# Kernel tuning notes

Hardware: AMD Instinct MI355X
Metric: run time of the kernel (lower is better)

The kernel has to match this reference:

```python
import jax, jax.numpy as jnp
import numpy as np
import math

D_MODEL = 1024
N_HEADS = 16
D_K = D_MODEL // N_HEADS
THRESH = 0.1  # attention probs below this are zeroed


def setup_inputs() -> dict:
    key = jax.random.key(0)
    ks = jax.random.split(key, 9)
    B, S, D = 2, 2048, D_MODEL
    scale = 1.0 / math.sqrt(D)
    x = jax.random.normal(ks[0], (B, S, D), dtype=jnp.float32)
    Wq = jax.random.normal(ks[1], (D, D), dtype=jnp.float32) * scale
    bq = jax.random.normal(ks[2], (D,), dtype=jnp.float32) * 0.01
    Wk = jax.random.normal(ks[3], (D, D), dtype=jnp.float32) * scale
    bk = jax.random.normal(ks[4], (D,), dtype=jnp.float32) * 0.01
    Wv = jax.random.normal(ks[5], (D, D), dtype=jnp.float32) * scale
    bv = jax.random.normal(ks[6], (D,), dtype=jnp.float32) * 0.01
    Wo = jax.random.normal(ks[7], (D, D), dtype=jnp.float32) * scale
    bo = jax.random.normal(ks[8], (D,), dtype=jnp.float32) * 0.01
    return {"x": x, "Wq": Wq, "bq": bq, "Wk": Wk, "bk": bk,
            "Wv": Wv, "bv": bv, "Wo": Wo, "bo": bo}


def _split_heads(t):
    B, S, D = t.shape
    return t.reshape(B, S, N_HEADS, D_K).transpose(0, 2, 1, 3)  # [B,H,S,dk]


def reference(x, Wq, bq, Wk, bk, Wv, bv, Wo, bo):
    # torch nn.Linear: y = x @ W.T + b
    q = _split_heads(x @ Wq.T + bq)
    k = _split_heads(x @ Wk.T + bk)
    v = _split_heads(x @ Wv.T + bv)
    scores = jnp.einsum('bhqd,bhkd->bhqk', q, k) / math.sqrt(D_K)
    probs = jax.nn.softmax(scores, axis=-1)          # full unmasked softmax (returned)
    keep = probs >= THRESH                            # ~low_attention_mask
    probs_model = jnp.where(keep, probs, 0.0)        # masked_fill; dropout is identity in eval
    ctx = jnp.einsum('bhqk,bhkd->bhqd', probs_model, v)
    B, H, S, dk = ctx.shape
    merged = ctx.transpose(0, 2, 1, 3).reshape(B, S, H * dk)
    out = merged @ Wo.T + bo
    attention_sum = probs.sum(axis=1)                # [B,S,S] sum over heads
    attention_mask = keep.astype(jnp.float32).sum(axis=1)  # [B,S,S]
    return (out, attention_sum, attention_mask)
```

## Files before the change

kernel.cpp:

```cpp
#include <hip/hip_runtime.h>

#define SDIM 2048
#define DDIM 1024
#define NH 16
#define DK 64
#define NB 2
#define MROWS (NB * SDIM)
#define MAXEV 65536
#define EXPC 0.18033688011112f
#define L01 -3.3219281f

typedef _Float16 f16x8 __attribute__((ext_vector_type(8)));
typedef _Float16 f16x4 __attribute__((ext_vector_type(4)));
typedef float f32x4 __attribute__((ext_vector_type(4)));

__device__ __forceinline__ void ld_lds16(const _Float16* g, _Float16* l) {
  __builtin_amdgcn_global_load_lds(
      (const __attribute__((address_space(1))) void*)g,
      (__attribute__((address_space(3))) void*)l, 16, 0, 0);
}

__global__ __launch_bounds__(256) void cvt_f16(
    const float* __restrict__ x, const float* __restrict__ wq,
    const float* __restrict__ wk, const float* __restrict__ wv,
    _Float16* __restrict__ xh, _Float16* __restrict__ wqh,
    _Float16* __restrict__ wkh, _Float16* __restrict__ wvh) {
  int i = blockIdx.x * 256 + threadIdx.x;
  const float* src;
  _Float16* dst;
  int off;
  if (i < 1048576) {
    src = x; dst = xh; off = i;
  } else if (i < 1310720) {
    src = wq; dst = wqh; off = i - 1048576;
  } else if (i < 1572864) {
    src = wk; dst = wkh; off = i - 1310720;
  } else {
    src = wv; dst = wvh; off = i - 1572864;
  }
  float4 v = ((const float4*)src)[off];
  f16x4 h;
  h[0] = (_Float16)v.x; h[1] = (_Float16)v.y;
  h[2] = (_Float16)v.z; h[3] = (_Float16)v.w;
  ((f16x4*)dst)[off] = h;
}

__global__ __launch_bounds__(256, 2) void proj_gemm(
    const _Float16* __restrict__ xh, const _Float16* __restrict__ Wqh,
    const _Float16* __restrict__ Wkh, const _Float16* __restrict__ Wvh,
    const float* __restrict__ bq, const float* __restrict__ bk,
    const float* __restrict__ bv, _Float16* __restrict__ Qo,
    _Float16* __restrict__ Ko, float* __restrict__ Vo) {
  __shared__ _Float16 sA[128 * 64];
  __shared__ _Float16 sB[128 * 64];
  const int t = threadIdx.x;
  const int lane = t & 63, wv = t >> 6;
  const int lr = lane & 15, quad = lane >> 4;
  const int wm = wv >> 1, wn = wv & 1;
  const int m0 = blockIdx.y * 128, n0 = blockIdx.x * 128;
  const int z = blockIdx.z;
  const _Float16* Bp = z == 0 ? Wqh : (z == 1 ? Wkh : Wvh);
  const float* bias = z == 0 ? bq : (z == 1 ? bk : bv);

  const int strow = t >> 3;
  const int stchunk = t & 7;
  const int stsrc = (stchunk ^ (strow & 7)) * 8;

  f32x4 acc[4][4];
#pragma unroll
  for (int i = 0; i < 4; ++i)
#pragma unroll
    for (int j = 0; j < 4; ++j) acc[i][j] = (f32x4){0.f, 0.f, 0.f, 0.f};

  for (int k0 = 0; k0 < DDIM; k0 += 64) {
    __syncthreads();
#pragma unroll
    for (int i = 0; i < 4; ++i) {
      const int row = i * 32 + strow;
      ld_lds16(&xh[(size_t)(m0 + row) * DDIM + k0 + stsrc],
               &sA[row * 64 + stchunk * 8]);
      ld_lds16(&Bp[(size_t)(n0 + row) * DDIM + k0 + stsrc],
               &sB[row * 64 + stchunk * 8]);
    }
    __syncthreads();
    f16x8 af[4][2], bf[4][2];
#pragma unroll
    for (int i = 0; i < 4; ++i)
#pragma unroll
      for (int kk = 0; kk < 2; ++kk) {
        const int ph = ((kk * 4 + quad) ^ (lr & 7)) * 8;
        af[i][kk] = *(const f16x8*)&sA[(wm * 64 + i * 16 + lr) * 64 + ph];
        bf[i][kk] = *(const f16x8*)&sB[(wn * 64 + i * 16 + lr) * 64 + ph];
      }
#pragma unroll
    for (int kk = 0; kk < 2; ++kk)
#pragma unroll
      for (int i = 0; i < 4; ++i)
#pragma unroll
        for (int j = 0; j < 4; ++j)
          acc[i][j] = __builtin_amdgcn_mfma_f32_16x16x32_f16(
              af[i][kk], bf[j][kk], acc[i][j], 0, 0, 0);
  }
#pragma unroll
  for (int j = 0; j < 4; ++j) {
    const int ng = n0 + wn * 64 + j * 16 + lr;
    const float bvv = bias[ng];
    const int h = ng >> 6, d = ng & 63;
#pragma unroll
    for (int i = 0; i < 4; ++i) {
#pragma unroll
      for (int r = 0; r < 4; ++r) {
        const int mg = m0 + wm * 64 + i * 16 + quad * 4 + r;
        const int b = mg >> 11, s = mg & 2047;
        const float o = acc[i][j][r] + bvv;
        const size_t off = ((size_t)(b * NH + h) * SDIM + s) * DK + d;
        if (z == 0)
          Qo[off] = (_Float16)(o * EXPC);
        else if (z == 1)
          Ko[off] = (_Float16)o;
        else
          Vo[off] = o;
      }
    }
  }
}

__global__ __launch_bounds__(256, 8) void attn_denom(
    const _Float16* __restrict__ Q, const _Float16* __restrict__ K,
    float* __restrict__ laOut) {
  __shared__ _Float16 KdA[64 * 64];
  __shared__ _Float16 KdB[64 * 64];
  const int t = threadIdx.x;
  const int lane = t & 63, wave = t >> 6;
  const int quad = lane >> 4, lr = lane & 15;
  const int id = blockIdx.x;
  const int xcd = id & 7, inner = id >> 3;
  const int bh = xcd * 4 + (inner >> 5);
  const int q0 = (inner & 31) * 64;
  const _Float16* Qh = Q + (size_t)bh * SDIM * DK;
  const _Float16* Kh = K + (size_t)bh * SDIM * DK;
  const size_t qoff = (size_t)(q0 + wave * 16 + lr) * DK + quad * 8;
  const f16x8 aq0 = *(const f16x8*)&Qh[qoff];
  const f16x8 aq1 = *(const f16x8*)&Qh[qoff + 32];
  const int strow = t >> 3, stchunk = t & 7;
  const int stsrc = (stchunk ^ (strow & 7)) * 8;
  const int ph0 = (quad ^ (lr & 7)) * 8;
  const int ph1 = ((4 + quad) ^ (lr & 7)) * 8;

#define STAGE_DN(KT, BUF)                                                  \
  {                                                                        \
    _Pragma("unroll") for (int i = 0; i < 2; ++i)                          \
        ld_lds16(&Kh[(size_t)((KT)*64 + i * 32 + strow) * DK + stsrc],     \
                 &BUF[(i * 32 + strow) * 64 + stchunk * 8]);               \
  }

#define COMPUTE_DN(BUF)                                                   \
  _Pragma("unroll") for (int c = 0; c < 4; ++c) {                         \
    f16x8 b0 = *(const f16x8*)&BUF[(c * 16 + lr) * 64 + ph0];             \
    f16x8 b1 = *(const f16x8*)&BUF[(c * 16 + lr) * 64 + ph1];             \
    f32x4 acc = {0.f, 0.f, 0.f, 0.f};                                     \
    acc = __builtin_amdgcn_mfma_f32_16x16x32_f16(aq0, b0, acc, 0, 0, 0);  \
    acc = __builtin_amdgcn_mfma_f32_16x16x32_f16(aq1, b1, acc, 0, 0, 0);  \
    _Pragma("unroll") for (int r = 0; r < 4; ++r)                         \
        dsum[r] += __builtin_amdgcn_exp2f(acc[r]);                        \
  }

  float dsum[4] = {0.f, 0.f, 0.f, 0.f};
  STAGE_DN(0, KdA);
#pragma unroll 1
  for (int kt = 0; kt < 32; kt += 2) {
    __syncthreads();
    STAGE_DN(kt + 1, KdB);
    COMPUTE_DN(KdA);
    __syncthreads();
    if (kt + 2 < 32) STAGE_DN(kt + 2, KdA);
    COMPUTE_DN(KdB);
  }
#pragma unroll
  for (int m = 1; m < 16; m <<= 1)
#pragma unroll
    for (int r = 0; r < 4; ++r)
      dsum[r] += __shfl_xor(dsum[r], m, 64);
  if (lr == 0) {
#pragma unroll
    for (int r = 0; r < 4; ++r)
      laOut[(size_t)bh * SDIM + q0 + wave * 16 + quad * 4 + r] =
          -__builtin_amdgcn_logf(dsum[r]);
  }
#undef STAGE_DN
#undef COMPUTE_DN
}

__global__ __launch_bounds__(256, 6) void attn_pass2(
    const _Float16* __restrict__ Q, const _Float16* __restrict__ K,
    const float* __restrict__ la, float* __restrict__ attSum,
    float* __restrict__ attMask, float4* __restrict__ ev,
    int* __restrict__ ecnt) {
  __shared__ __align__(16) float SMEM[64 * 68];
  _Float16* KbufA = (_Float16*)SMEM;
  _Float16* KbufB = (_Float16*)SMEM + 4096;
  float* Tbuf = SMEM;
  const int t = threadIdx.x;
  const int lane = t & 63, wave = t >> 6;
  const int quad = lane >> 4, lr = lane & 15;
  const int id = blockIdx.x;
  const int xcd = id & 7, inner = id >> 3;
  const int b = xcd >> 2;
  const int q0 = (((xcd >> 1) & 1) * 16 + (inner >> 4)) * 64;
  const int k0 = ((xcd & 1) * 16 + (inner & 15)) * 64;
  const int strow = t >> 3, stchunk = t & 7;
  const int stsrc = (stchunk ^ (strow & 7)) * 8;
  const int ph0 = (quad ^ (lr & 7)) * 8;
  const int ph1 = ((4 + quad) ^ (lr & 7)) * 8;

  const size_t qbase = ((size_t)(b * NH) * SDIM + q0 + wave * 16 + lr) * DK;
  const size_t dbase = (size_t)(b * NH) * SDIM + q0 + wave * 16 + quad * 4;
  const size_t hstep = (size_t)SDIM * DK;

  float asum[4][4] = {};
  float mxr[4] = {-1e30f, -1e30f, -1e30f, -1e30f};

  f16x8 aq0c, aq1c, aq0n, aq1n;
  float4 lavc, lavn;

#define STAGE_H(H, BUF)                                                      \
  {                                                                          \
    const _Float16* Kp =                                                     \
        K + (size_t)(b * NH + (H)) * hstep + (size_t)k0 * DK;                \
    _Pragma("unroll") for (int i = 0; i < 2; ++i)                            \
        ld_lds16(&Kp[(size_t)(i * 32 + strow) * DK + stsrc],                 \
                 &BUF[(i * 32 + strow) * 64 + stchunk * 8]);                 \
  }

#define LOADQ_H(H, A0, A1, LV)                                               \
  {                                                                          \
    const size_t ho = (size_t)(H)*hstep;                                     \
    A0 = *(const f16x8*)&Q[qbase + ho + quad * 8];                           \
    A1 = *(const f16x8*)&Q[qbase + ho + 32 + quad * 8];                      \
    LV = *(const float4*)&la[dbase + (size_t)(H)*SDIM];                      \
  }

#define COMPUTE_H(BUF, A0, A1, LV)                                           \
  {                                                                          \
    const float lar[4] = {LV.x, LV.y, LV.z, LV.w};                           \
    _Pragma("unroll") for (int c = 0; c < 4; ++c) {                          \
      f16x8 b0 = *(const f16x8*)&BUF[(c * 16 + lr) * 64 + ph0];              \
      f16x8 b1 = *(const f16x8*)&BUF[(c * 16 + lr) * 64 + ph1];              \
      f32x4 acc = {0.f, 0.f, 0.f, 0.f};                                      \
      acc = __builtin_amdgcn_mfma_f32_16x16x32_f16(A0, b0, acc, 0, 0, 0);    \
      acc = __builtin_amdgcn_mfma_f32_16x16x32_f16(A1, b1, acc, 0, 0, 0);    \
      _Pragma("unroll") for (int r = 0; r < 4; ++r) {                        \
        const float arg = acc[r] + lar[r];                                   \
        mxr[r] = fmaxf(mxr[r], arg);                                         \
        asum[c][r] += __builtin_amdgcn_exp2f(arg);                           \
      }                                                                      \
    }                                                                        \
  }

  STAGE_H(0, KbufA);
  LOADQ_H(0, aq0c, aq1c, lavc);
#pragma unroll 1
  for (int h = 0; h < NH; h += 2) {
    __syncthreads();
    STAGE_H(h + 1, KbufB);
    LOADQ_H(h + 1, aq0n, aq1n, lavn);
    COMPUTE_H(KbufA, aq0c, aq1c, lavc);
    __syncthreads();
    if (h + 2 < NH) {
      STAGE_H(h + 2, KbufA);
      LOADQ_H(h + 2, aq0c, aq1c, lavc);
    }
    COMPUTE_H(KbufB, aq0n, aq1n, lavn);
  }
#undef STAGE_H
#undef LOADQ_H
#undef COMPUTE_H

  const float mx =
      fmaxf(fmaxf(mxr[0], mxr[1]), fmaxf(mxr[2], mxr[3]));
  if (__any(mx >= L01)) {
    float amask[4][4] = {};
#pragma unroll 1
    for (int h = 0; h < NH; ++h) {
      const _Float16* Kp =
          K + (size_t)(b * NH + h) * hstep + (size_t)k0 * DK;
      const size_t ho = (size_t)h * hstep;
      const f16x8 aq0 = *(const f16x8*)&Q[qbase + ho + quad * 8];
      const f16x8 aq1 = *(const f16x8*)&Q[qbase + ho + 32 + quad * 8];
      const float4 l4 = *(const float4*)&la[dbase + (size_t)h * SDIM];
      const float lar[4] = {l4.x, l4.y, l4.z, l4.w};
#pragma unroll 1
      for (int c = 0; c < 4; ++c) {
        const f16x8 b0 = *(const f16x8*)&Kp[(c * 16 + lr) * DK + quad * 8];
        const f16x8 b1 = *(const f16x8*)&Kp[(c * 16 + lr) * DK + 32 + quad * 8];
        f32x4 acc = {0.f, 0.f, 0.f, 0.f};
        acc = __builtin_amdgcn_mfma_f32_16x16x32_f16(aq0, b0, acc, 0, 0, 0);
        acc = __builtin_amdgcn_mfma_f32_16x16x32_f16(aq1, b1, acc, 0, 0, 0);
#pragma unroll 1
        for (int r = 0; r < 4; ++r) {
          const float p = __builtin_amdgcn_exp2f(acc[r] + lar[r]);
          if (p >= 0.1f) {
            amask[c][r] += 1.0f;
            int idx = atomicAdd(ecnt, 1);
            if (idx < MAXEV)
              ev[idx] = make_float4(
                  __int_as_float(b * NH + h),
                  __int_as_float(q0 + wave * 16 + quad * 4 + r),
                  __int_as_float(k0 + c * 16 + lr), p);
          }
        }
      }
    }
#pragma unroll
    for (int c = 0; c < 4; ++c)
#pragma unroll
      for (int r = 0; r < 4; ++r)
        if (amask[c][r] != 0.0f) {
          const size_t row = (size_t)(b * SDIM) + q0 + wave * 16 + quad * 4 + r;
          attMask[row * SDIM + k0 + c * 16 + lr] = amask[c][r];
        }
  }
  const int g8 = t >> 3;
  const int l8 = (t & 7) * 4;
  __syncthreads();
#pragma unroll
  for (int c = 0; c < 4; ++c)
#pragma unroll
    for (int r = 0; r < 4; ++r)
      Tbuf[(wave * 16 + quad * 4 + r) * 68 + c * 16 + lr] = asum[c][r];
  __syncthreads();
#pragma unroll
  for (int p = 0; p < 2; ++p)
#pragma unroll
    for (int qh = 0; qh < 2; ++qh) {
      const int row = p * 32 + g8, col = qh * 32 + l8;
      f32x4 v = *(const f32x4*)&Tbuf[row * 68 + col];
      __builtin_nontemporal_store(
          v, (f32x4*)&attSum[((size_t)(b * SDIM) + q0 + row) * SDIM + k0 + col]);
    }
}

__global__ __launch_bounds__(64) void apply_events(
    const float4* __restrict__ ev, const int* __restrict__ ecnt,
    const float* __restrict__ V, float* __restrict__ merged,
    int* __restrict__ flags) {
  int n = *ecnt;
  if (n > MAXEV) n = MAXEV;
  const int d = threadIdx.x;
  for (int e = blockIdx.x; e < n; e += gridDim.x) {
    float4 r = ev[e];
    int bh = __float_as_int(r.x);
    int q = __float_as_int(r.y);
    int kc = __float_as_int(r.z);
    float p = r.w;
    int b = bh >> 4, h = bh & 15;
    atomicAdd(&merged[((size_t)(b * SDIM + q)) * DDIM + h * DK + d],
              p * V[((size_t)bh * SDIM + kc) * DK + d]);
    if (d == 0) flags[b * SDIM + q] = 1;
  }
}

__global__ __launch_bounds__(256) void out_gemm(const float* __restrict__ A,
                                                const float* __restrict__ W,
                                                const float* __restrict__ bias,
                                                float* __restrict__ out,
                                                const int* __restrict__ flags) {
  __shared__ float As[16][68];
  __shared__ float Ws[16][68];
  __shared__ int anyF;
  const int t = threadIdx.x;
  const int tx = t & 15, ty = t >> 4;
  const int m0 = blockIdx.y * 64;
  const int n0 = blockIdx.x * 64;
  if (t == 0) anyF = 0;
  __syncthreads();
  if (t < 64 && flags[m0 + t]) anyF = 1;
  __syncthreads();
  const int nb = n0 + tx * 4;
  const float4 bv = *(const float4*)&bias[nb];
  if (!anyF) {
#pragma unroll
    for (int r = 0; r < 4; ++r)
      *(float4*)&out[(size_t)(m0 + ty * 4 + r) * DDIM + nb] = bv;
    return;
  }
  const int lr = t >> 2;
  const int lc = (t & 3) * 4;
  float acc[4][4] = {};
  for (int k0 = 0; k0 < DDIM; k0 += 16) {
    __syncthreads();
    float4 av = *(const float4*)&A[(size_t)(m0 + lr) * DDIM + k0 + lc];
    float4 wv = *(const float4*)&W[(size_t)(n0 + lr) * DDIM + k0 + lc];
    As[lc + 0][lr] = av.x; As[lc + 1][lr] = av.y;
    As[lc + 2][lr] = av.z; As[lc + 3][lr] = av.w;
    Ws[lc + 0][lr] = wv.x; Ws[lc + 1][lr] = wv.y;
    Ws[lc + 2][lr] = wv.z; Ws[lc + 3][lr] = wv.w;
    __syncthreads();
#pragma unroll
    for (int kk = 0; kk < 16; ++kk) {
      float4 a4 = *(const float4*)&As[kk][ty * 4];
      float4 b4 = *(const float4*)&Ws[kk][tx * 4];
      const float a[4] = {a4.x, a4.y, a4.z, a4.w};
      const float b[4] = {b4.x, b4.y, b4.z, b4.w};
#pragma unroll
      for (int r = 0; r < 4; ++r)
#pragma unroll
        for (int c = 0; c < 4; ++c)
          acc[r][c] = fmaf(a[r], b[c], acc[r][c]);
    }
  }
#pragma unroll
  for (int r = 0; r < 4; ++r) {
    float4 o;
    o.x = acc[r][0] + bv.x;
    o.y = acc[r][1] + bv.y;
    o.z = acc[r][2] + bv.z;
    o.w = acc[r][3] + bv.w;
    *(float4*)&out[(size_t)(m0 + ty * 4 + r) * DDIM + nb] = o;
  }
}

extern "C" void kernel_launch(void* const* d_in, const int* in_sizes, int n_in,
                              void* d_out, int out_size, void* d_ws,
                              size_t ws_size, hipStream_t stream) {
  const float* x = (const float*)d_in[0];
  const float* Wq = (const float*)d_in[1];
  const float* bq = (const float*)d_in[2];
  const float* Wk = (const float*)d_in[3];
  const float* bk = (const float*)d_in[4];
  const float* Wv = (const float*)d_in[5];
  const float* bv = (const float*)d_in[6];
  const float* Wo = (const float*)d_in[7];
  const float* bo = (const float*)d_in[8];

  float* out = (float*)d_out;
  float* attSum = out + (size_t)MROWS * DDIM;
  float* attMask = attSum + (size_t)NB * SDIM * SDIM;

  char* ws = (char*)d_ws;
  const size_t bigF = (size_t)MROWS * DDIM * sizeof(float);
  const size_t bigH = (size_t)MROWS * DDIM * sizeof(_Float16);
  const size_t wH = (size_t)DDIM * DDIM * sizeof(_Float16);
  _Float16* Qh = (_Float16*)ws;  ws += bigH;
  _Float16* Kh = (_Float16*)ws;  ws += bigH;
  float* V = (float*)ws;         ws += bigF;
  float* merged = (float*)ws;    ws += bigF;
  _Float16* xh = (_Float16*)ws;  ws += bigH;
  _Float16* Wqh = (_Float16*)ws; ws += wH;
  _Float16* Wkh = (_Float16*)ws; ws += wH;
  _Float16* Wvh = (_Float16*)ws; ws += wH;
  float* laBuf = (float*)ws;     ws += (size_t)NB * NH * SDIM * sizeof(float);
  float4* ev = (float4*)ws;      ws += (size_t)MAXEV * sizeof(float4);
  int* flags = (int*)ws;         ws += (size_t)MROWS * sizeof(int);
  int* ecnt = (int*)ws;          ws += 16;

  hipMemsetAsync(merged, 0, bigF, stream);
  hipMemsetAsync(flags, 0, (size_t)MROWS * sizeof(int), stream);
  hipMemsetAsync(ecnt, 0, 16, stream);
  hipMemsetAsync(attMask, 0, (size_t)NB * SDIM * SDIM * sizeof(float), stream);

  dim3 blk(256);
  cvt_f16<<<dim3(7168), blk, 0, stream>>>(x, Wq, Wk, Wv, xh, Wqh, Wkh, Wvh);
  proj_gemm<<<dim3(8, 32, 3), blk, 0, stream>>>(xh, Wqh, Wkh, Wvh, bq, bk, bv,
                                                Qh, Kh, V);
  attn_denom<<<dim3(1024), blk, 0, stream>>>(Qh, Kh, laBuf);
  attn_pass2<<<dim3(2048), blk, 0, stream>>>(Qh, Kh, laBuf, attSum,
                                             attMask, ev, ecnt);
  apply_events<<<dim3(256), dim3(64), 0, stream>>>(ev, ecnt, V, merged, flags);
  out_gemm<<<dim3(16, 64), blk, 0, stream>>>(merged, Wo, bo, out, flags);
}
```

Before: 267.8 us.

## Load K fragments directly from global memory instead of LDS double-buffering

In attn_denom and attn_pass2, the LDS double-buffered K staging (global_load_lds plus swizzled LDS reads and two barriers per iteration) is removed. Each wave now loads its K MFMA fragments straight from global memory into registers, relying on L1/L2 for reuse across the block's four waves. Occupancy hints drop to 4 blocks per CU so more registers are available for prefetching. This removes barrier and LDS traffic, but each block now issues redundant global loads and relies on cache hits and on unrolling for latency hiding.

Measured after the change: 427.1 us. +59.5%, slower.

```diff
diff --git a/kernel.cpp b/kernel.cpp
--- a/kernel.cpp
+++ b/kernel.cpp
@@ -125,11 +125,9 @@
   }
 }
 
-__global__ __launch_bounds__(256, 8) void attn_denom(
+__global__ __launch_bounds__(256, 4) void attn_denom(
     const _Float16* __restrict__ Q, const _Float16* __restrict__ K,
     float* __restrict__ laOut) {
-  __shared__ _Float16 KdA[64 * 64];
-  __shared__ _Float16 KdB[64 * 64];
   const int t = threadIdx.x;
   const int lane = t & 63, wave = t >> 6;
   const int quad = lane >> 4, lr = lane & 15;
@@ -142,39 +140,26 @@
   const size_t qoff = (size_t)(q0 + wave * 16 + lr) * DK + quad * 8;
   const f16x8 aq0 = *(const f16x8*)&Qh[qoff];
   const f16x8 aq1 = *(const f16x8*)&Qh[qoff + 32];
-  const int strow = t >> 3, stchunk = t & 7;
-  const int stsrc = (stchunk ^ (strow & 7)) * 8;
-  const int ph0 = (quad ^ (lr & 7)) * 8;
-  const int ph1 = ((4 + quad) ^ (lr & 7)) * 8;
-
-#define STAGE_DN(KT, BUF)                                                  \
-  {                                                                        \
-    _Pragma("unroll") for (int i = 0; i < 2; ++i)                          \
-        ld_lds16(&Kh[(size_t)((KT)*64 + i * 32 + strow) * DK + stsrc],     \
-                 &BUF[(i * 32 + strow) * 64 + stchunk * 8]);               \
-  }
-
-#define COMPUTE_DN(BUF)                                                   \
-  _Pragma("unroll") for (int c = 0; c < 4; ++c) {                         \
-    f16x8 b0 = *(const f16x8*)&BUF[(c * 16 + lr) * 64 + ph0];             \
-    f16x8 b1 = *(const f16x8*)&BUF[(c * 16 + lr) * 64 + ph1];             \
-    f32x4 acc = {0.f, 0.f, 0.f, 0.f};                                     \
-    acc = __builtin_amdgcn_mfma_f32_16x16x32_f16(aq0, b0, acc, 0, 0, 0);  \
-    acc = __builtin_amdgcn_mfma_f32_16x16x32_f16(aq1, b1, acc, 0, 0, 0);  \
-    _Pragma("unroll") for (int r = 0; r < 4; ++r)                         \
-        dsum[r] += __builtin_amdgcn_exp2f(acc[r]);                        \
-  }
 
   float dsum[4] = {0.f, 0.f, 0.f, 0.f};
-  STAGE_DN(0, KdA);
-#pragma unroll 1
-  for (int kt = 0; kt < 32; kt += 2) {
-    __syncthreads();
-    STAGE_DN(kt + 1, KdB);
-    COMPUTE_DN(KdA);
-    __syncthreads();
-    if (kt + 2 < 32) STAGE_DN(kt + 2, KdA);
-    COMPUTE_DN(KdB);
+#pragma unroll 2
+  for (int kt = 0; kt < 32; ++kt) {
+    const _Float16* Kp = Kh + (size_t)kt * 64 * DK;
+    f16x8 b0[4], b1[4];
+#pragma unroll
+    for (int c = 0; c < 4; ++c) {
+      b0[c] = *(const f16x8*)&Kp[(c * 16 + lr) * DK + quad * 8];
+      b1[c] = *(const f16x8*)&Kp[(c * 16 + lr) * DK + 32 + quad * 8];
+    }
+#pragma unroll
+    for (int c = 0; c < 4; ++c) {
+      f32x4 acc = {0.f, 0.f, 0.f, 0.f};
+      acc = __builtin_amdgcn_mfma_f32_16x16x32_f16(aq0, b0[c], acc, 0, 0, 0);
+      acc = __builtin_amdgcn_mfma_f32_16x16x32_f16(aq1, b1[c], acc, 0, 0, 0);
+#pragma unroll
+      for (int r = 0; r < 4; ++r)
+        dsum[r] += __builtin_amdgcn_exp2f(acc[r]);
+    }
   }
 #pragma unroll
   for (int m = 1; m < 16; m <<= 1)
@@ -187,19 +172,14 @@
       laOut[(size_t)bh * SDIM + q0 + wave * 16 + quad * 4 + r] =
           -__builtin_amdgcn_logf(dsum[r]);
   }
-#undef STAGE_DN
-#undef COMPUTE_DN
-}
-
-__global__ __launch_bounds__(256, 6) void attn_pass2(
+}
+
+__global__ __launch_bounds__(256, 4) void attn_pass2(
     const _Float16* __restrict__ Q, const _Float16* __restrict__ K,
     const float* __restrict__ la, float* __restrict__ attSum,
     float* __restrict__ attMask, float4* __restrict__ ev,
     int* __restrict__ ecnt) {
-  __shared__ __align__(16) float SMEM[64 * 68];
-  _Float16* KbufA = (_Float16*)SMEM;
-  _Float16* KbufB = (_Float16*)SMEM + 4096;
-  float* Tbuf = SMEM;
+  __shared__ __align__(16) float Tbuf[64 * 68];
   const int t = threadIdx.x;
   const int lane = t & 63, wave = t >> 6;
   const int quad = lane >> 4, lr = lane & 15;
@@ -208,10 +188,6 @@
   const int b = xcd >> 2;
   const int q0 = (((xcd >> 1) & 1) * 16 + (inner >> 4)) * 64;
   const int k0 = ((xcd & 1) * 16 + (inner & 15)) * 64;
-  const int strow = t >> 3, stchunk = t & 7;
-  const int stsrc = (stchunk ^ (strow & 7)) * 8;
-  const int ph0 = (quad ^ (lr & 7)) * 8;
-  const int ph1 = ((4 + quad) ^ (lr & 7)) * 8;
 
   const size_t qbase = ((size_t)(b * NH) * SDIM + q0 + wave * 16 + lr) * DK;
   const size_t dbase = (size_t)(b * NH) * SDIM + q0 + wave * 16 + quad * 4;
@@ -220,61 +196,33 @@
   float asum[4][4] = {};
   float mxr[4] = {-1e30f, -1e30f, -1e30f, -1e30f};
 
-  f16x8 aq0c, aq1c, aq0n, aq1n;
-  float4 lavc, lavn;
-
-#define STAGE_H(H, BUF)                                                      \
-  {                                                                          \
-    const _Float16* Kp =                                                     \
-        K + (size_t)(b * NH + (H)) * hstep + (size_t)k0 * DK;                \
-    _Pragma("unroll") for (int i = 0; i < 2; ++i)                            \
-        ld_lds16(&Kp[(size_t)(i * 32 + strow) * DK + stsrc],                 \
-                 &BUF[(i * 32 + strow) * 64 + stchunk * 8]);                 \
-  }
-
-#define LOADQ_H(H, A0, A1, LV)                                               \
-  {                                                                          \
-    const size_t ho = (size_t)(H)*hstep;                                     \
-    A0 = *(const f16x8*)&Q[qbase + ho + quad * 8];                           \
-    A1 = *(const f16x8*)&Q[qbase + ho + 32 + quad * 8];                      \
-    LV = *(const float4*)&la[dbase + (size_t)(H)*SDIM];                      \
-  }
-
-#define COMPUTE_H(BUF, A0, A1, LV)                                           \
-  {                                                                          \
-    const float lar[4] = {LV.x, LV.y, LV.z, LV.w};                           \
-    _Pragma("unroll") for (int c = 0; c < 4; ++c) {                          \
-      f16x8 b0 = *(const f16x8*)&BUF[(c * 16 + lr) * 64 + ph0];              \
-      f16x8 b1 = *(const f16x8*)&BUF[(c * 16 + lr) * 64 + ph1];              \
-      f32x4 acc = {0.f, 0.f, 0.f, 0.f};                                      \
-      acc = __builtin_amdgcn_mfma_f32_16x16x32_f16(A0, b0, acc, 0, 0, 0);    \
-      acc = __builtin_amdgcn_mfma_f32_16x16x32_f16(A1, b1, acc, 0, 0, 0);    \
-      _Pragma("unroll") for (int r = 0; r < 4; ++r) {                        \
-        const float arg = acc[r] + lar[r];                                   \
-        mxr[r] = fmaxf(mxr[r], arg);                                         \
-        asum[c][r] += __builtin_amdgcn_exp2f(arg);                           \
-      }                                                                      \
-    }                                                                        \
-  }
-
-  STAGE_H(0, KbufA);
-  LOADQ_H(0, aq0c, aq1c, lavc);
-#pragma unroll 1
-  for (int h = 0; h < NH; h += 2) {
-    __syncthreads();
-    STAGE_H(h + 1, KbufB);
-    LOADQ_H(h + 1, aq0n, aq1n, lavn);
-    COMPUTE_H(KbufA, aq0c, aq1c, lavc);
-    __syncthreads();
-    if (h + 2 < NH) {
-      STAGE_H(h + 2, KbufA);
-      LOADQ_H(h + 2, aq0c, aq1c, lavc);
-    }
-    COMPUTE_H(KbufB, aq0n, aq1n, lavn);
-  }
-#undef STAGE_H
-#undef LOADQ_H
-#undef COMPUTE_H
+#pragma unroll 2
+  for (int h = 0; h < NH; ++h) {
+    const _Float16* Kp = K + (size_t)(b * NH + h) * hstep + (size_t)k0 * DK;
+    const size_t ho = (size_t)h * hstep;
+    const f16x8 aq0 = *(const f16x8*)&Q[qbase + ho + quad * 8];
+    const f16x8 aq1 = *(const f16x8*)&Q[qbase + ho + 32 + quad * 8];
+    const float4 l4 = *(const float4*)&la[dbase + (size_t)h * SDIM];
+    const float lar[4] = {l4.x, l4.y, l4.z, l4.w};
+    f16x8 b0[4], b1[4];
+#pragma unroll
+    for (int c = 0; c < 4; ++c) {
+      b0[c] = *(const f16x8*)&Kp[(c * 16 + lr) * DK + quad * 8];
+      b1[c] = *(const f16x8*)&Kp[(c * 16 + lr) * DK + 32 + quad * 8];
+    }
+#pragma unroll
+    for (int c = 0; c < 4; ++c) {
+      f32x4 acc = {0.f, 0.f, 0.f, 0.f};
+      acc = __builtin_amdgcn_mfma_f32_16x16x32_f16(aq0, b0[c], acc, 0, 0, 0);
+      acc = __builtin_amdgcn_mfma_f32_16x16x32_f16(aq1, b1[c], acc, 0, 0, 0);
+#pragma unroll
+      for (int r = 0; r < 4; ++r) {
+        const float arg = acc[r] + lar[r];
+        mxr[r] = fmaxf(mxr[r], arg);
+        asum[c][r] += __builtin_amdgcn_exp2f(arg);
+      }
+    }
+  }
 
   const float mx =
       fmaxf(fmaxf(mxr[0], mxr[1]), fmaxf(mxr[2], mxr[3]));
@@ -322,7 +270,6 @@
   }
   const int g8 = t >> 3;
   const int l8 = (t & 7) * 4;
-  __syncthreads();
 #pragma unroll
   for (int c = 0; c < 4; ++c)
 #pragma unroll
```

## Use triple-buffered K staging with partial vmcnt waits and single barrier

Applied to the files above, without the earlier changes.

Both attention kernels switch from double-buffered K tiles with two __syncthreads per pair of iterations to a three-slot ring buffer with one barrier per iteration. Each barrier is preceded by a partial s_waitcnt vmcnt, so the prefetch for the next tile can stay in flight while the current tile is computed. The aim is to hide global-to-LDS load latency and cut barrier overhead. In exchange, LDS use grows and attn_denom's occupancy hint drops from 8 to 6. Correctness now depends on the hand-counted vmcnt values matching the number of outstanding loads.

After: 254.2 us. 5.1% less time.

```diff
diff --git a/kernel.cpp b/kernel.cpp
--- a/kernel.cpp
+++ b/kernel.cpp
@@ -125,11 +125,10 @@
   }
 }
 
-__global__ __launch_bounds__(256, 8) void attn_denom(
+__global__ __launch_bounds__(256, 6) void attn_denom(
     const _Float16* __restrict__ Q, const _Float16* __restrict__ K,
     float* __restrict__ laOut) {
-  __shared__ _Float16 KdA[64 * 64];
-  __shared__ _Float16 KdB[64 * 64];
+  __shared__ __align__(16) _Float16 KS[3 * 4096];
   const int t = threadIdx.x;
   const int lane = t & 63, wave = t >> 6;
   const int quad = lane >> 4, lr = lane & 15;
@@ -151,13 +150,13 @@
   {                                                                        \
     _Pragma("unroll") for (int i = 0; i < 2; ++i)                          \
         ld_lds16(&Kh[(size_t)((KT)*64 + i * 32 + strow) * DK + stsrc],     \
-                 &BUF[(i * 32 + strow) * 64 + stchunk * 8]);               \
+                 &(BUF)[(i * 32 + strow) * 64 + stchunk * 8]);             \
   }
 
 #define COMPUTE_DN(BUF)                                                   \
   _Pragma("unroll") for (int c = 0; c < 4; ++c) {                         \
-    f16x8 b0 = *(const f16x8*)&BUF[(c * 16 + lr) * 64 + ph0];             \
-    f16x8 b1 = *(const f16x8*)&BUF[(c * 16 + lr) * 64 + ph1];             \
+    f16x8 b0 = *(const f16x8*)&(BUF)[(c * 16 + lr) * 64 + ph0];           \
+    f16x8 b1 = *(const f16x8*)&(BUF)[(c * 16 + lr) * 64 + ph1];           \
     f32x4 acc = {0.f, 0.f, 0.f, 0.f};                                     \
     acc = __builtin_amdgcn_mfma_f32_16x16x32_f16(aq0, b0, acc, 0, 0, 0);  \
     acc = __builtin_amdgcn_mfma_f32_16x16x32_f16(aq1, b1, acc, 0, 0, 0);  \
@@ -166,15 +165,21 @@
   }
 
   float dsum[4] = {0.f, 0.f, 0.f, 0.f};
-  STAGE_DN(0, KdA);
+  STAGE_DN(0, KS);
+  int cb = 0;
 #pragma unroll 1
-  for (int kt = 0; kt < 32; kt += 2) {
-    __syncthreads();
-    STAGE_DN(kt + 1, KdB);
-    COMPUTE_DN(KdA);
-    __syncthreads();
-    if (kt + 2 < 32) STAGE_DN(kt + 2, KdA);
-    COMPUTE_DN(KdB);
+  for (int kt = 0; kt < 32; ++kt) {
+    const int nb_ = cb == 2 ? 0 : cb + 1;
+    if (kt + 1 < 32) STAGE_DN(kt + 1, KS + nb_ * 4096);
+    asm volatile("" ::: "memory");
+    if (kt + 1 < 32)
+      asm volatile("s_waitcnt vmcnt(2)" ::: "memory");
+    else
+      asm volatile("s_waitcnt vmcnt(0)" ::: "memory");
+    __builtin_amdgcn_s_barrier();
+    asm volatile("" ::: "memory");
+    COMPUTE_DN(KS + cb * 4096);
+    cb = nb_;
   }
 #pragma unroll
   for (int m = 1; m < 16; m <<= 1)
@@ -196,10 +201,8 @@
     const float* __restrict__ la, float* __restrict__ attSum,
     float* __restrict__ attMask, float4* __restrict__ ev,
     int* __restrict__ ecnt) {
-  __shared__ __align__(16) float SMEM[64 * 68];
-  _Float16* KbufA = (_Float16*)SMEM;
-  _Float16* KbufB = (_Float16*)SMEM + 4096;
-  float* Tbuf = SMEM;
+  __shared__ __align__(16) _Float16 KS[3 * 4096];
+  float* Tbuf = (float*)KS;
   const int t = threadIdx.x;
   const int lane = t & 63, wave = t >> 6;
   const int quad = lane >> 4, lr = lane & 15;
@@ -220,7 +223,7 @@
   float asum[4][4] = {};
   float mxr[4] = {-1e30f, -1e30f, -1e30f, -1e30f};
 
-  f16x8 aq0c, aq1c, aq0n, aq1n;
+  f16x8 a0c, a1c, a0n, a1n;
   float4 lavc, lavn;
 
 #define STAGE_H(H, BUF)                                                      \
@@ -229,7 +232,7 @@
         K + (size_t)(b * NH + (H)) * hstep + (size_t)k0 * DK;                \
     _Pragma("unroll") for (int i = 0; i < 2; ++i)                            \
         ld_lds16(&Kp[(size_t)(i * 32 + strow) * DK + stsrc],                 \
-                 &BUF[(i * 32 + strow) * 64 + stchunk * 8]);                 \
+                 &(BUF)[(i * 32 + strow) * 64 + stchunk * 8]);               \
   }
 
 #define LOADQ_H(H, A0, A1, LV)                                               \
@@ -244,8 +247,8 @@
   {                                                                          \
     const float lar[4] = {LV.x, LV.y, LV.z, LV.w};                           \
     _Pragma("unroll") for (int c = 0; c < 4; ++c) {                          \
-      f16x8 b0 = *(const f16x8*)&BUF[(c * 16 + lr) * 64 + ph0];              \
-      f16x8 b1 = *(const f16x8*)&BUF[(c * 16 + lr) * 64 + ph1];              \
+      f16x8 b0 = *(const f16x8*)&(BUF)[(c * 16 + lr) * 64 + ph0];            \
+      f16x8 b1 = *(const f16x8*)&(BUF)[(c * 16 + lr) * 64 + ph1];            \
       f32x4 acc = {0.f, 0.f, 0.f, 0.f};                                      \
       acc = __builtin_amdgcn_mfma_f32_16x16x32_f16(A0, b0, acc, 0, 0, 0);    \
       acc = __builtin_amdgcn_mfma_f32_16x16x32_f16(A1, b1, acc, 0, 0, 0);    \
@@ -257,20 +260,28 @@
     }                                                                        \
   }
 
-  STAGE_H(0, KbufA);
-  LOADQ_H(0, aq0c, aq1c, lavc);
+  STAGE_H(0, KS);
+  LOADQ_H(0, a0c, a1c, lavc);
+  int cb = 0;
 #pragma unroll 1
-  for (int h = 0; h < NH; h += 2) {
-    __syncthreads();
-    STAGE_H(h + 1, KbufB);
-    LOADQ_H(h + 1, aq0n, aq1n, lavn);
-    COMPUTE_H(KbufA, aq0c, aq1c, lavc);
-    __syncthreads();
-    if (h + 2 < NH) {
-      STAGE_H(h + 2, KbufA);
-      LOADQ_H(h + 2, aq0c, aq1c, lavc);
-    }
-    COMPUTE_H(KbufB, aq0n, aq1n, lavn);
+  for (int h = 0; h < NH; ++h) {
+    const int nb_ = cb == 2 ? 0 : cb + 1;
+    if (h + 1 < NH) {
+      STAGE_H(h + 1, KS + nb_ * 4096);
+      LOADQ_H(h + 1, a0n, a1n, lavn);
+    }
+    asm volatile("" ::: "memory");
+    if (h + 1 < NH)
+      asm volatile("s_waitcnt vmcnt(5)" ::: "memory");
+    else
+      asm volatile("s_waitcnt vmcnt(0)" ::: "memory");
+    __builtin_amdgcn_s_barrier();
+    asm volatile("" ::: "memory");
+    COMPUTE_H(KS + cb * 4096, a0c, a1c, lavc);
+    if (h + 1 < NH) {
+      a0c = a0n; a1c = a1n; lavc = lavn;
+    }
+    cb = nb_;
   }
 #undef STAGE_H
 #undef LOADQ_H
```

## Give each wave private K tiles to drop block barriers in attention passes

Applied to the files above, without the earlier changes.

Each of the four waves now stages its own full copy of the 64x64 K tile into a private double-buffered LDS region, and waits on its own loads with explicit vmcnt counters instead of block-wide __syncthreads. This removes inter-wave barrier stalls in attn_denom and attn_pass2. The log-denominator is also folded into the MFMA accumulator init, which saves an add. The cost is four times the LDS footprint and four times the K global loads per block, and occupancy hints drop from 8 and 6 to 2, so latency hiding may suffer. The hand-written vmcnt values must exactly match the issued load counts, or the waves will read stale tiles.

Result: slower. 288.0 us (+7.5%).

```diff
diff --git a/kernel.cpp b/kernel.cpp
--- a/kernel.cpp
+++ b/kernel.cpp
@@ -125,11 +125,10 @@
   }
 }
 
-__global__ __launch_bounds__(256, 8) void attn_denom(
+__global__ __launch_bounds__(256, 2) void attn_denom(
     const _Float16* __restrict__ Q, const _Float16* __restrict__ K,
     float* __restrict__ laOut) {
-  __shared__ _Float16 KdA[64 * 64];
-  __shared__ _Float16 KdB[64 * 64];
+  __shared__ __align__(16) _Float16 KS[4 * 2 * 4096];
   const int t = threadIdx.x;
   const int lane = t & 63, wave = t >> 6;
   const int quad = lane >> 4, lr = lane & 15;
@@ -142,22 +141,25 @@
   const size_t qoff = (size_t)(q0 + wave * 16 + lr) * DK + quad * 8;
   const f16x8 aq0 = *(const f16x8*)&Qh[qoff];
   const f16x8 aq1 = *(const f16x8*)&Qh[qoff + 32];
-  const int strow = t >> 3, stchunk = t & 7;
-  const int stsrc = (stchunk ^ (strow & 7)) * 8;
+  const int srow8 = lane >> 3;
+  const int scol = ((lane & 7) ^ srow8) * 8;
   const int ph0 = (quad ^ (lr & 7)) * 8;
   const int ph1 = ((4 + quad) ^ (lr & 7)) * 8;
-
-#define STAGE_DN(KT, BUF)                                                  \
+  _Float16* W0 = &KS[wave * 8192];
+  _Float16* W1 = W0 + 4096;
+
+#define STAGE_DW(KT, BUF)                                                  \
   {                                                                        \
-    _Pragma("unroll") for (int i = 0; i < 2; ++i)                          \
-        ld_lds16(&Kh[(size_t)((KT)*64 + i * 32 + strow) * DK + stsrc],     \
-                 &BUF[(i * 32 + strow) * 64 + stchunk * 8]);               \
+    const _Float16* Kp = Kh + (size_t)(KT)*64 * DK;                        \
+    _Pragma("unroll") for (int i = 0; i < 8; ++i)                          \
+        ld_lds16(&Kp[(size_t)(i * 8 + srow8) * DK + scol],                 \
+                 &(BUF)[i * 512 + lane * 8]);                              \
   }
 
 #define COMPUTE_DN(BUF)                                                   \
   _Pragma("unroll") for (int c = 0; c < 4; ++c) {                         \
-    f16x8 b0 = *(const f16x8*)&BUF[(c * 16 + lr) * 64 + ph0];             \
-    f16x8 b1 = *(const f16x8*)&BUF[(c * 16 + lr) * 64 + ph1];             \
+    f16x8 b0 = *(const f16x8*)&(BUF)[(c * 16 + lr) * 64 + ph0];           \
+    f16x8 b1 = *(const f16x8*)&(BUF)[(c * 16 + lr) * 64 + ph1];           \
     f32x4 acc = {0.f, 0.f, 0.f, 0.f};                                     \
     acc = __builtin_amdgcn_mfma_f32_16x16x32_f16(aq0, b0, acc, 0, 0, 0);  \
     acc = __builtin_amdgcn_mfma_f32_16x16x32_f16(aq1, b1, acc, 0, 0, 0);  \
@@ -166,15 +168,21 @@
   }
 
   float dsum[4] = {0.f, 0.f, 0.f, 0.f};
-  STAGE_DN(0, KdA);
+  STAGE_DW(0, W0);
 #pragma unroll 1
   for (int kt = 0; kt < 32; kt += 2) {
-    __syncthreads();
-    STAGE_DN(kt + 1, KdB);
-    COMPUTE_DN(KdA);
-    __syncthreads();
-    if (kt + 2 < 32) STAGE_DN(kt + 2, KdA);
-    COMPUTE_DN(KdB);
+    STAGE_DW(kt + 1, W1);
+    asm volatile("s_waitcnt vmcnt(8)" ::: "memory");
+    __builtin_amdgcn_sched_barrier(0);
+    COMPUTE_DN(W0);
+    if (kt + 2 < 32) {
+      STAGE_DW(kt + 2, W0);
+      asm volatile("s_waitcnt vmcnt(8)" ::: "memory");
+    } else {
+      asm volatile("s_waitcnt vmcnt(0)" ::: "memory");
+    }
+    __builtin_amdgcn_sched_barrier(0);
+    COMPUTE_DN(W1);
   }
 #pragma unroll
   for (int m = 1; m < 16; m <<= 1)
@@ -187,19 +195,17 @@
       laOut[(size_t)bh * SDIM + q0 + wave * 16 + quad * 4 + r] =
           -__builtin_amdgcn_logf(dsum[r]);
   }
-#undef STAGE_DN
+#undef STAGE_DW
 #undef COMPUTE_DN
 }
 
-__global__ __launch_bounds__(256, 6) void attn_pass2(
+__global__ __launch_bounds__(256, 2) void attn_pass2(
     const _Float16* __restrict__ Q, const _Float16* __restrict__ K,
     const float* __restrict__ la, float* __restrict__ attSum,
     float* __restrict__ attMask, float4* __restrict__ ev,
     int* __restrict__ ecnt) {
-  __shared__ __align__(16) float SMEM[64 * 68];
-  _Float16* KbufA = (_Float16*)SMEM;
-  _Float16* KbufB = (_Float16*)SMEM + 4096;
-  float* Tbuf = SMEM;
+  __shared__ __align__(16) _Float16 KS[4 * 2 * 4096];
+  float* Tbuf = (float*)KS;
   const int t = threadIdx.x;
   const int lane = t & 63, wave = t >> 6;
   const int quad = lane >> 4, lr = lane & 15;
@@ -208,10 +214,12 @@
   const int b = xcd >> 2;
   const int q0 = (((xcd >> 1) & 1) * 16 + (inner >> 4)) * 64;
   const int k0 = ((xcd & 1) * 16 + (inner & 15)) * 64;
-  const int strow = t >> 3, stchunk = t & 7;
-  const int stsrc = (stchunk ^ (strow & 7)) * 8;
+  const int srow8 = lane >> 3;
+  const int scol = ((lane & 7) ^ srow8) * 8;
   const int ph0 = (quad ^ (lr & 7)) * 8;
   const int ph1 = ((4 + quad) ^ (lr & 7)) * 8;
+  _Float16* W0 = &KS[wave * 8192];
+  _Float16* W1 = W0 + 4096;
 
   const size_t qbase = ((size_t)(b * NH) * SDIM + q0 + wave * 16 + lr) * DK;
   const size_t dbase = (size_t)(b * NH) * SDIM + q0 + wave * 16 + quad * 4;
@@ -220,19 +228,19 @@
   float asum[4][4] = {};
   float mxr[4] = {-1e30f, -1e30f, -1e30f, -1e30f};
 
-  f16x8 aq0c, aq1c, aq0n, aq1n;
-  float4 lavc, lavn;
-
-#define STAGE_H(H, BUF)                                                      \
+  f16x8 a0A, a1A, a0B, a1B;
+  float4 lavA, lavB;
+
+#define STAGE_W(H, BUF)                                                      \
   {                                                                          \
     const _Float16* Kp =                                                     \
         K + (size_t)(b * NH + (H)) * hstep + (size_t)k0 * DK;                \
-    _Pragma("unroll") for (int i = 0; i < 2; ++i)                            \
-        ld_lds16(&Kp[(size_t)(i * 32 + strow) * DK + stsrc],                 \
-                 &BUF[(i * 32 + strow) * 64 + stchunk * 8]);                 \
-  }
-
-#define LOADQ_H(H, A0, A1, LV)                                               \
+    _Pragma("unroll") for (int i = 0; i < 8; ++i)                            \
+        ld_lds16(&Kp[(size_t)(i * 8 + srow8) * DK + scol],                   \
+                 &(BUF)[i * 512 + lane * 8]);                                \
+  }
+
+#define LOADQ_W(H, A0, A1, LV)                                               \
   {                                                                          \
     const size_t ho = (size_t)(H)*hstep;                                     \
     A0 = *(const f16x8*)&Q[qbase + ho + quad * 8];                           \
@@ -240,41 +248,44 @@
     LV = *(const float4*)&la[dbase + (size_t)(H)*SDIM];                      \
   }
 
-#define COMPUTE_H(BUF, A0, A1, LV)                                           \
+#define COMPUTE_W(BUF, A0, A1, LV)                                           \
   {                                                                          \
-    const float lar[4] = {LV.x, LV.y, LV.z, LV.w};                           \
     _Pragma("unroll") for (int c = 0; c < 4; ++c) {                          \
-      f16x8 b0 = *(const f16x8*)&BUF[(c * 16 + lr) * 64 + ph0];              \
-      f16x8 b1 = *(const f16x8*)&BUF[(c * 16 + lr) * 64 + ph1];              \
-      f32x4 acc = {0.f, 0.f, 0.f, 0.f};                                      \
+      f16x8 b0 = *(const f16x8*)&(BUF)[(c * 16 + lr) * 64 + ph0];            \
+      f16x8 b1 = *(const f16x8*)&(BUF)[(c * 16 + lr) * 64 + ph1];            \
+      f32x4 acc = {LV.x, LV.y, LV.z, LV.w};             \
       acc = __builtin_amdgcn_mfma_f32_16x16x32_f16(A0, b0, acc, 0, 0, 0);    \
       acc = __builtin_amdgcn_mfma_f32_16x16x32_f16(A1, b1, acc, 0, 0, 0);    \
       _Pragma("unroll") for (int r = 0; r < 4; ++r) {                        \
-        const float arg = acc[r] + lar[r];                                   \
+        const float arg = acc[r];                                            \
         mxr[r] = fmaxf(mxr[r], arg);                                         \
         asum[c][r] += __builtin_amdgcn_exp2f(arg);                           \
       }                                                                      \
     }                                                                        \
   }
 
-  STAGE_H(0, KbufA);
-  LOADQ_H(0, aq0c, aq1c, lavc);
+  STAGE_W(0, W0);
+  LOADQ_W(0, a0A, a1A, lavA);
 #pragma unroll 1
   for (int h = 0; h < NH; h += 2) {
-    __syncthreads();
-    STAGE_H(h + 1, KbufB);
-    LOADQ_H(h + 1, aq0n, aq1n, lavn);
-    COMPUTE_H(KbufA, aq0c, aq1c, lavc);
-    __syncthreads();
+    STAGE_W(h + 1, W1);
+    LOADQ_W(h + 1, a0B, a1B, lavB);
+    asm volatile("s_waitcnt vmcnt(11)" ::: "memory");
+    __builtin_amdgcn_sched_barrier(0);
+    COMPUTE_W(W0, a0A, a1A, lavA);
     if (h + 2 < NH) {
-      STAGE_H(h + 2, KbufA);
-      LOADQ_H(h + 2, aq0c, aq1c, lavc);
-    }
-    COMPUTE_H(KbufB, aq0n, aq1n, lavn);
-  }
-#undef STAGE_H
-#undef LOADQ_H
-#undef COMPUTE_H
+      STAGE_W(h + 2, W0);
+      LOADQ_W(h + 2, a0A, a1A, lavA);
+      asm volatile("s_waitcnt vmcnt(11)" ::: "memory");
+    } else {
+      asm volatile("s_waitcnt vmcnt(0)" ::: "memory");
+    }
+    __builtin_amdgcn_sched_barrier(0);
+    COMPUTE_W(W1, a0B, a1B, lavB);
+  }
+#undef STAGE_W
+#undef LOADQ_W
+#undef COMPUTE_W
 
   const float mx =
       fmaxf(fmaxf(mxr[0], mxr[1]), fmaxf(mxr[2], mxr[3]));
```
